# Kernel optimization log

Measured on AMD Instinct MI355X. Metric: run time of the kernel, lower is better.

Reference implementation:

```python
import jax, jax.numpy as jnp
import numpy as np
import math

A, R, E, H = 4, 2, 12, 24  # msg_angular, msg_radial, embed_dim, hidden_dim
N = A * R
B, L = 131072, 15

def _ring_adj(n):
    adj = np.zeros((n, n), np.float32)
    if n == 1:
        adj[0, 0] = 1.0
    else:
        for i in range(n):
            adj[i, (i - 1) % n] = 1.0
            adj[i, (i + 1) % n] = 1.0
    return jnp.asarray(adj)

ANG_ADJ = _ring_adj(A)
RAD_ADJ = _ring_adj(R)

def setup_inputs():
    key = jax.random.key(0)
    ks = jax.random.split(key, 16)
    p = lambda k, s: jax.random.normal(k, s, jnp.float32) * 0.1
    return {
        "x": jax.random.normal(ks[0], (B, L, 4), jnp.float32),
        "enc_w1": p(ks[1], (4, H)), "enc_b1": p(ks[2], (H,)),
        "enc_w2": p(ks[3], (H, H)), "enc_b2": p(ks[4], (H,)),
        "enc_w3": p(ks[5], (H, 3)), "enc_b3": p(ks[6], (3,)),
        "node_w1": p(ks[7], (E, H)), "node_b1": p(ks[8], (H,)),
        "node_w2": p(ks[9], (H, E)), "node_b2": p(ks[10], (E,)),
        "angular_logit": jnp.zeros((A,), jnp.float32),
        "radial_logit": jnp.zeros((R,), jnp.float32),
        "read_w1": p(ks[11], (E * N, H)), "read_b1": p(ks[12], (H,)),
        "read_w2": p(ks[13], (H, 4)), "read_b2": p(ks[14], (4,)),
    }

def _norm_adj(logit, adj):
    a = jax.nn.softmax(logit)[None, :] * adj
    return a / jnp.maximum(a.sum(1, keepdims=True), 1e-6)

def _forward(x, enc_w1, enc_b1, enc_w2, enc_b2, enc_w3, enc_b3,
             node_w1, node_b1, node_w2, node_b2,
             angular_logit, radial_logit,
             read_w1, read_b1, read_w2, read_b2):
    b = x.shape[0]
    # encoder: original loops over all timesteps but only uses the last z
    zt = jnp.tanh(x[:, -1, :] @ enc_w1 + enc_b1)
    zt = jnp.tanh(zt @ enc_w2 + enc_b2)
    z = zt @ enc_w3 + enc_b3                       # [B, 3]
    r = jax.nn.sigmoid(z[:, 0]) * (R - 1)          # R_idx in [0, R-1]
    p = (z[:, 1] + math.pi) / (2 * math.pi) * A    # phi_idx (can be <0 or >A)
    # torch code calls .item(), detaching indices/weights from autograd
    r = jax.lax.stop_gradient(r)
    p = jax.lax.stop_gradient(p)
    r0 = jnp.trunc(r)   # int() truncates toward zero
    p0 = jnp.trunc(p)
    dr = (r - r0)[:, None]
    dp = (p - p0)[:, None]
    dro = jnp.array([0.0, 0.0, 1.0, 1.0], jnp.float32)   # 4 bilinear corners
    dpo = jnp.array([0.0, 1.0, 0.0, 1.0], jnp.float32)
    wr = jnp.where(dro == 0, 1.0 - dr, dr)               # [B, 4]
    wp = jnp.where(dpo == 0, 1.0 - dp, dp)
    w = wr * wp                                          # [B, 4]
    r_i = jnp.minimum(r0.astype(jnp.int32)[:, None] + dro.astype(jnp.int32), R - 1)
    p_i = jnp.mod(p0.astype(jnp.int32)[:, None] + dpo.astype(jnp.int32), A)
    mask = (w > 0).astype(x.dtype)[:, :, None]           # 'if weight > 0' skip
    # node_embed = pad(concat([z, weight]), E); z entries are NOT weight-scaled
    vec = jnp.concatenate([
        jnp.broadcast_to(z[:, None, :], (b, 4, 3)),
        w[:, :, None],
        jnp.zeros((b, 4, E - 4), x.dtype)], axis=-1) * mask   # [B, 4, E]
    grid = jnp.zeros((b, R, A, E), x.dtype).at[
        jnp.arange(b)[:, None], r_i, p_i].add(vec)            # scatter-add
    h = grid.reshape(b, N, E)
    ang = _norm_adj(angular_logit, ANG_ADJ)  # [A, A]
    rad = _norm_adj(radial_logit, RAD_ADJ)   # [R, R]
    # faithful to the torch .view() layout mixing (r,a,e)
    h_ang = jnp.einsum('ij,bjk->bik', ang, h.reshape(b, A, R * E)).reshape(b, N, E)
    h_rad = jnp.einsum('ij,bjk->bik', rad, h.reshape(b, R, A * E)).reshape(b, N, E)
    h = h + h_ang + h_rad
    h = jnp.tanh(h @ node_w1 + node_b1) @ node_w2 + node_b2   # node_net
    out = jnp.tanh(h.reshape(b, -1) @ read_w1 + read_b1) @ read_w2 + read_b2
    return out  # [B, 4]

def reference(x, enc_w1, enc_b1, enc_w2, enc_b2, enc_w3, enc_b3,
              node_w1, node_b1, node_w2, node_b2,
              angular_logit, radial_logit,
              read_w1, read_b1, read_w2, read_b2):
    return _forward(x, enc_w1, enc_b1, enc_w2, enc_b2, enc_w3, enc_b3,
                    node_w1, node_b1, node_w2, node_b2,
                    angular_logit, radial_logit,
                    read_w1, read_b1, read_w2, read_b2)
```

## Files before the change

kernel.cpp:

```cpp
#include <hip/hip_runtime.h>
#include <math.h>


#define PI_F 3.14159265358979323846f

__device__ __forceinline__ float fast_tanh(float v) {
    float e = __expf(2.0f * v);
    return 1.0f - 2.0f * __builtin_amdgcn_rcpf(e + 1.0f);
}

__device__ __forceinline__ float quad_sum(float x) {
    x += __int_as_float(__builtin_amdgcn_update_dpp(
             0, __float_as_int(x), 0xB1, 0xF, 0xF, true));
    x += __int_as_float(__builtin_amdgcn_update_dpp(
             0, __float_as_int(x), 0x4E, 0xF, 0xF, true));
    return x;
}

#define K1_LDS 880

extern "C" __global__ void __launch_bounds__(256, 2)
topo_k1(const float* __restrict__ x,
        const float* __restrict__ ew1, const float* __restrict__ eb1,
        const float* __restrict__ ew2, const float* __restrict__ eb2,
        const float* __restrict__ ew3, const float* __restrict__ eb3,
        const float* __restrict__ alog, const float* __restrict__ rlog,
        const float* __restrict__ nw2, const float* __restrict__ nb2,
        const float* __restrict__ rw1, const float* __restrict__ rb1,
        float* __restrict__ ws, int B)
{
    const int nb1b = (B + 255) >> 8;

    if ((int)blockIdx.x >= nb1b) {
        const int gid = ((int)blockIdx.x - nb1b) * 256 + (int)threadIdx.x;
        float* M = ws + (size_t)B * 20;
        if (gid < 4608) {
            const int cell = gid / 576, rem = gid - cell * 576;
            const int j = rem / 24, j2 = rem - j * 24;
            float s = 0.0f;
            #pragma unroll
            for (int d = 0; d < 12; ++d)
                s += nw2[j * 12 + d] * rw1[(cell * 12 + d) * 24 + j2];
            M[gid] = s;
        } else if (gid < 4632) {
            const int j2 = gid - 4608;
            float s = rb1[j2];
            for (int i = 0; i < 96; ++i)
                s += nb2[i % 12] * rw1[i * 24 + j2];
            M[4608 + j2] = s;
        }
        return;
    }

    __shared__ float wf[K1_LDS];
    const float4* wq = reinterpret_cast<const float4*>(wf);
    {
        const int tt = threadIdx.x;
        for (int i = tt; i < 24; i += 256) {
            wf[i * 8 + 0] = ew1[i];
            wf[i * 8 + 1] = ew1[24 + i];
            wf[i * 8 + 2] = ew1[48 + i];
            wf[i * 8 + 3] = ew1[72 + i];
            wf[i * 8 + 4] = eb1[i];
        }
        for (int i = tt; i < 576; i += 256) wf[192 + i] = ew2[i];
        for (int i = tt; i < 24;  i += 256) wf[768 + i] = eb2[i];
        for (int i = tt; i < 72;  i += 256) wf[792 + (i % 3) * 24 + (i / 3)] = ew3[i];
        for (int i = tt; i < 3;   i += 256) wf[864 + i] = eb3[i];
    }
    __syncthreads();

    const int b = blockIdx.x * blockDim.x + threadIdx.x;
    if (b >= B) return;

    const float4 xv = *reinterpret_cast<const float4*>(x + (size_t)b * 60 + 56);

    float a2[24];
    #pragma unroll
    for (int c = 0; c < 6; ++c) {
        float4 b4 = wq[192 / 4 + c];
        a2[c*4+0] = b4.x; a2[c*4+1] = b4.y; a2[c*4+2] = b4.z; a2[c*4+3] = b4.w;
    }
    #pragma unroll 1
    for (int k = 0; k < 24; ++k) {
        float4 p  = wq[2 * k];
        float4 p2 = wq[2 * k + 1];
        const float zk = fast_tanh(p2.x + xv.x*p.x + xv.y*p.y + xv.z*p.z + xv.w*p.w);
        const int rr = 48 + k * 6;
        float4 r0 = wq[rr+0], r1 = wq[rr+1], r2 = wq[rr+2];
        float4 r3 = wq[rr+3], r4 = wq[rr+4], r5 = wq[rr+5];
        a2[0]+=zk*r0.x; a2[1]+=zk*r0.y; a2[2]+=zk*r0.z; a2[3]+=zk*r0.w;
        a2[4]+=zk*r1.x; a2[5]+=zk*r1.y; a2[6]+=zk*r1.z; a2[7]+=zk*r1.w;
        a2[8]+=zk*r2.x; a2[9]+=zk*r2.y; a2[10]+=zk*r2.z; a2[11]+=zk*r2.w;
        a2[12]+=zk*r3.x; a2[13]+=zk*r3.y; a2[14]+=zk*r3.z; a2[15]+=zk*r3.w;
        a2[16]+=zk*r4.x; a2[17]+=zk*r4.y; a2[18]+=zk*r4.z; a2[19]+=zk*r4.w;
        a2[20]+=zk*r5.x; a2[21]+=zk*r5.y; a2[22]+=zk*r5.z; a2[23]+=zk*r5.w;
    }
    float zt2[24];
    #pragma unroll
    for (int j = 0; j < 24; ++j) zt2[j] = fast_tanh(a2[j]);

    float z0 = wf[864], z1 = wf[865], z2 = wf[866];
    #pragma unroll
    for (int c = 0; c < 6; ++c) {
        float4 v0 = wq[198 + c], v1 = wq[204 + c], v2 = wq[210 + c];
        z0 += zt2[c*4+0]*v0.x + zt2[c*4+1]*v0.y + zt2[c*4+2]*v0.z + zt2[c*4+3]*v0.w;
        z1 += zt2[c*4+0]*v1.x + zt2[c*4+1]*v1.y + zt2[c*4+2]*v1.z + zt2[c*4+3]*v1.w;
        z2 += zt2[c*4+0]*v2.x + zt2[c*4+1]*v2.y + zt2[c*4+2]*v2.z + zt2[c*4+3]*v2.w;
    }

    float ang[4][4];
    {
        float m = fmaxf(fmaxf(alog[0], alog[1]), fmaxf(alog[2], alog[3]));
        float e0 = __expf(alog[0] - m), e1 = __expf(alog[1] - m);
        float e2 = __expf(alog[2] - m), e3 = __expf(alog[3] - m);
        float s = e0 + e1 + e2 + e3;
        float sm[4] = { e0 / s, e1 / s, e2 / s, e3 / s };
        #pragma unroll
        for (int i = 0; i < 4; ++i) {
            const int jn = (i + 3) & 3, jp = (i + 1) & 3;
            float inv = 1.0f / fmaxf(sm[jn] + sm[jp], 1e-6f);
            #pragma unroll
            for (int j = 0; j < 4; ++j) {
                float adj = (j == jn || j == jp) ? 1.0f : 0.0f;
                ang[i][j] = sm[j] * adj * inv;
            }
        }
    }
    float rad[2][2];
    {
        float m = fmaxf(rlog[0], rlog[1]);
        float f0 = __expf(rlog[0] - m), f1 = __expf(rlog[1] - m);
        float fs = f0 + f1;
        float sm0 = f0 / fs, sm1 = f1 / fs;
        rad[0][0] = 0.0f; rad[0][1] = sm1 / fmaxf(sm1, 1e-6f);
        rad[1][1] = 0.0f; rad[1][0] = sm0 / fmaxf(sm0, 1e-6f);
    }

    const float r = 1.0f / (1.0f + __expf(-z0));
    const float p = (z1 + PI_F) / (2.0f * PI_F) * 4.0f;
    const float r0f = truncf(r), p0f = truncf(p);
    const float dr = r - r0f, dp = p - p0f;
    const int r0i = (int)r0f, p0i = (int)p0f;

    const float w0c = (1.0f - dr) * (1.0f - dp);
    const float w1c = (1.0f - dr) * dp;
    const float w2c = dr * (1.0f - dp);
    const float w3c = dr * dp;

    const int ri0 = min(r0i, 1);
    const int ri2 = min(r0i + 1, 1);
    const int pi0 = p0i & 3;
    const int pi1 = (p0i + 1) & 3;

    const int c0 = ri0 * 4 + pi0, c1 = ri0 * 4 + pi1;
    const int c2 = ri2 * 4 + pi0, c3 = ri2 * 4 + pi1;

    float cnt[8], wsum[8];
    #pragma unroll
    for (int n = 0; n < 8; ++n) {
        float cm = 0.0f, cw = 0.0f;
        if (c0 == n && w0c > 0.0f) { cm += 1.0f; cw += w0c; }
        if (c1 == n && w1c > 0.0f) { cm += 1.0f; cw += w1c; }
        if (c2 == n && w2c > 0.0f) { cm += 1.0f; cw += w2c; }
        if (c3 == n && w3c > 0.0f) { cm += 1.0f; cw += w3c; }
        cnt[n] = cm; wsum[n] = cw;
    }
    float mc[8], mw[8];
    #pragma unroll
    for (int n = 0; n < 8; ++n) {
        float ac = cnt[n], aw = wsum[n];
        #pragma unroll
        for (int j = 0; j < 4; ++j) {
            const float g = ang[n >> 1][j];
            ac += g * cnt[2 * j + (n & 1)];
            aw += g * wsum[2 * j + (n & 1)];
        }
        #pragma unroll
        for (int j = 0; j < 2; ++j) {
            const float g = rad[n >> 2][j];
            ac += g * cnt[4 * j + (n & 3)];
            aw += g * wsum[4 * j + (n & 3)];
        }
        mc[n] = ac; mw[n] = aw;
    }

    float* wp = ws + (size_t)b * 20;
    float4 v0; v0.x = z0;    v0.y = z1;    v0.z = z2;    v0.w = 0.0f;
    float4 v1; v1.x = mc[0]; v1.y = mc[1]; v1.z = mc[2]; v1.w = mc[3];
    float4 v2; v2.x = mc[4]; v2.y = mc[5]; v2.z = mc[6]; v2.w = mc[7];
    float4 v3; v3.x = mw[0]; v3.y = mw[1]; v3.z = mw[2]; v3.w = mw[3];
    float4 v4; v4.x = mw[4]; v4.y = mw[5]; v4.z = mw[6]; v4.w = mw[7];
    reinterpret_cast<float4*>(wp)[0] = v0;
    reinterpret_cast<float4*>(wp)[1] = v1;
    reinterpret_cast<float4*>(wp)[2] = v2;
    reinterpret_cast<float4*>(wp)[3] = v3;
    reinterpret_cast<float4*>(wp)[4] = v4;
}

#define K2_LDS 4956

extern "C" __global__ void __launch_bounds__(256)
topo_k2(const float* __restrict__ ws,
        const float* __restrict__ nw1, const float* __restrict__ nb1,
        const float* __restrict__ rw2, const float* __restrict__ rb2,
        float* __restrict__ out, int B)
{
    __shared__ float wf[K2_LDS];
    const float4* wq = reinterpret_cast<const float4*>(wf);
    {
        const int tt = threadIdx.x;
        const float* Msrc = ws + (size_t)B * 20;
        for (int i = tt; i < 4608; i += 256) {
            const int cell = i / 576, rem = i - cell * 576;
            wf[192 + cell * 580 + rem] = Msrc[i];
        }
        for (int i = tt; i < 24; i += 256) wf[4832 + i] = Msrc[4608 + i];
        for (int i = tt; i < 24; i += 256) {
            wf[i * 8 + 0] = nw1[i];
            wf[i * 8 + 1] = nw1[24 + i];
            wf[i * 8 + 2] = nw1[48 + i];
            wf[i * 8 + 3] = nw1[72 + i];
            wf[i * 8 + 4] = nb1[i];
        }
        for (int i = tt; i < 96; i += 256) wf[4856 + i] = rw2[i];
        for (int i = tt; i < 4;  i += 256) wf[4952 + i] = rb2[i];
    }
    __syncthreads();

    const int tid  = blockIdx.x * blockDim.x + threadIdx.x;
    const int lane = tid & 3;
    const int b    = tid >> 2;
    if (b >= B) return;

    const float* wp = ws + (size_t)b * 20;
    const float4 zv = *reinterpret_cast<const float4*>(wp);
    const float2 mc2 = *reinterpret_cast<const float2*>(wp + 4 + 2 * lane);
    const float2 mw2 = *reinterpret_cast<const float2*>(wp + 12 + 2 * lane);
    const float z0 = zv.x, z1 = zv.y, z2 = zv.z;
    const float mcA = mc2.x, mcB = mc2.y, mwA = mw2.x, mwB = mw2.y;

    const int mAq = 48 + (2 * lane) * 145;
    const int mBq = mAq + 145;

    float t[24];
    #pragma unroll
    for (int j = 0; j < 24; ++j) t[j] = 0.0f;

    #pragma unroll 1
    for (int j = 0; j < 24; ++j) {
        float4 pk  = wq[2 * j];
        float4 pk2 = wq[2 * j + 1];
        const float q  = z0 * pk.x + z1 * pk.y + z2 * pk.z;
        const float hA = fast_tanh(pk2.x + mcA * q + mwA * pk.w);
        const float hB = fast_tanh(pk2.x + mcB * q + mwB * pk.w);
        const int ra = mAq + j * 6, rb = mBq + j * 6;
        float4 a0 = wq[ra+0], a1 = wq[ra+1], a2v = wq[ra+2];
        float4 a3 = wq[ra+3], a4 = wq[ra+4], a5  = wq[ra+5];
        float4 b0 = wq[rb+0], b1 = wq[rb+1], b2v = wq[rb+2];
        float4 b3 = wq[rb+3], b4 = wq[rb+4], b5  = wq[rb+5];
        t[0]  += hA*a0.x  + hB*b0.x;  t[1]  += hA*a0.y  + hB*b0.y;
        t[2]  += hA*a0.z  + hB*b0.z;  t[3]  += hA*a0.w  + hB*b0.w;
        t[4]  += hA*a1.x  + hB*b1.x;  t[5]  += hA*a1.y  + hB*b1.y;
        t[6]  += hA*a1.z  + hB*b1.z;  t[7]  += hA*a1.w  + hB*b1.w;
        t[8]  += hA*a2v.x + hB*b2v.x; t[9]  += hA*a2v.y + hB*b2v.y;
        t[10] += hA*a2v.z + hB*b2v.z; t[11] += hA*a2v.w + hB*b2v.w;
        t[12] += hA*a3.x  + hB*b3.x;  t[13] += hA*a3.y  + hB*b3.y;
        t[14] += hA*a3.z  + hB*b3.z;  t[15] += hA*a3.w  + hB*b3.w;
        t[16] += hA*a4.x  + hB*b4.x;  t[17] += hA*a4.y  + hB*b4.y;
        t[18] += hA*a4.z  + hB*b4.z;  t[19] += hA*a4.w  + hB*b4.w;
        t[20] += hA*a5.x  + hB*b5.x;  t[21] += hA*a5.y  + hB*b5.y;
        t[22] += hA*a5.z  + hB*b5.z;  t[23] += hA*a5.w  + hB*b5.w;
    }

    #pragma unroll
    for (int j = 0; j < 24; ++j) t[j] = quad_sum(t[j]) + wf[4832 + j];

    float4 ob = wq[1238];
    float o0 = ob.x, o1 = ob.y, o2 = ob.z, o3 = ob.w;
    #pragma unroll
    for (int j = 0; j < 24; ++j) {
        const float tv = fast_tanh(t[j]);
        float4 rv = wq[1214 + j];
        o0 += tv * rv.x; o1 += tv * rv.y; o2 += tv * rv.z; o3 += tv * rv.w;
    }
    if (lane == 0) {
        float4 ov; ov.x = o0; ov.y = o1; ov.z = o2; ov.w = o3;
        *reinterpret_cast<float4*>(out + (size_t)b * 4) = ov;
    }
}

extern "C" __global__ void __launch_bounds__(256, 2)
topo_fused(const float* __restrict__ x,
           const float* __restrict__ ew1, const float* __restrict__ eb1,
           const float* __restrict__ ew2, const float* __restrict__ eb2,
           const float* __restrict__ ew3, const float* __restrict__ eb3,
           const float* __restrict__ nw1, const float* __restrict__ nb1,
           const float* __restrict__ nw2, const float* __restrict__ nb2,
           const float* __restrict__ alog, const float* __restrict__ rlog,
           const float* __restrict__ rw1, const float* __restrict__ rb1,
           const float* __restrict__ rw2, const float* __restrict__ rb2,
           float* __restrict__ out, int B)
{
    const int b = blockIdx.x * blockDim.x + threadIdx.x;
    if (b >= B) return;

    float ang[4][4];
    {
        float m = fmaxf(fmaxf(alog[0], alog[1]), fmaxf(alog[2], alog[3]));
        float e0 = __expf(alog[0] - m), e1 = __expf(alog[1] - m);
        float e2 = __expf(alog[2] - m), e3 = __expf(alog[3] - m);
        float s = e0 + e1 + e2 + e3;
        float sm[4] = { e0 / s, e1 / s, e2 / s, e3 / s };
        #pragma unroll
        for (int i = 0; i < 4; ++i) {
            const int jn = (i + 3) & 3, jp = (i + 1) & 3;
            float inv = 1.0f / fmaxf(sm[jn] + sm[jp], 1e-6f);
            #pragma unroll
            for (int j = 0; j < 4; ++j) {
                float adj = (j == jn || j == jp) ? 1.0f : 0.0f;
                ang[i][j] = sm[j] * adj * inv;
            }
        }
    }
    float rad[2][2];
    {
        float m = fmaxf(rlog[0], rlog[1]);
        float f0 = __expf(rlog[0] - m), f1 = __expf(rlog[1] - m);
        float fs = f0 + f1;
        float sm0 = f0 / fs, sm1 = f1 / fs;
        rad[0][0] = 0.0f; rad[0][1] = sm1 / fmaxf(sm1, 1e-6f);
        rad[1][1] = 0.0f; rad[1][0] = sm0 / fmaxf(sm0, 1e-6f);
    }

    const float4 xv = *reinterpret_cast<const float4*>(x + (size_t)b * 60 + 56);
    float zt[24];
    #pragma unroll
    for (int j = 0; j < 24; ++j) {
        float a = eb1[j];
        a += xv.x * ew1[j];
        a += xv.y * ew1[24 + j];
        a += xv.z * ew1[48 + j];
        a += xv.w * ew1[72 + j];
        zt[j] = fast_tanh(a);
    }
    float z0 = eb3[0], z1 = eb3[1], z2 = eb3[2];
    #pragma unroll
    for (int j = 0; j < 24; ++j) {
        float a = eb2[j];
        #pragma unroll
        for (int k = 0; k < 24; ++k) a += zt[k] * ew2[k * 24 + j];
        const float z2t = fast_tanh(a);
        z0 += z2t * ew3[j * 3 + 0];
        z1 += z2t * ew3[j * 3 + 1];
        z2 += z2t * ew3[j * 3 + 2];
    }

    const float r = 1.0f / (1.0f + __expf(-z0));
    const float p = (z1 + PI_F) / (2.0f * PI_F) * 4.0f;
    const float r0f = truncf(r), p0f = truncf(p);
    const float dr = r - r0f, dp = p - p0f;
    const int r0i = (int)r0f, p0i = (int)p0f;
    const float w0c = (1.0f - dr) * (1.0f - dp);
    const float w1c = (1.0f - dr) * dp;
    const float w2c = dr * (1.0f - dp);
    const float w3c = dr * dp;
    const int ri0 = min(r0i, 1);
    const int ri2 = min(r0i + 1, 1);
    const int pi0 = p0i & 3;
    const int pi1 = (p0i + 1) & 3;
    const int c0 = ri0 * 4 + pi0, c1 = ri0 * 4 + pi1;
    const int c2 = ri2 * 4 + pi0, c3 = ri2 * 4 + pi1;

    float cnt[8], wsum[8];
    #pragma unroll
    for (int n = 0; n < 8; ++n) {
        float cm = 0.0f, cw = 0.0f;
        if (c0 == n && w0c > 0.0f) { cm += 1.0f; cw += w0c; }
        if (c1 == n && w1c > 0.0f) { cm += 1.0f; cw += w1c; }
        if (c2 == n && w2c > 0.0f) { cm += 1.0f; cw += w2c; }
        if (c3 == n && w3c > 0.0f) { cm += 1.0f; cw += w3c; }
        cnt[n] = cm; wsum[n] = cw;
    }
    float mc[8], mw[8];
    #pragma unroll
    for (int n = 0; n < 8; ++n) {
        float ac = cnt[n], aw = wsum[n];
        #pragma unroll
        for (int j = 0; j < 4; ++j) {
            const float g = ang[n >> 1][j];
            ac += g * cnt[2 * j + (n & 1)];
            aw += g * wsum[2 * j + (n & 1)];
        }
        #pragma unroll
        for (int j = 0; j < 2; ++j) {
            const float g = rad[n >> 2][j];
            ac += g * cnt[4 * j + (n & 3)];
            aw += g * wsum[4 * j + (n & 3)];
        }
        mc[n] = ac; mw[n] = aw;
    }

    float t[24];
    #pragma unroll
    for (int j = 0; j < 24; ++j) t[j] = rb1[j];
    #pragma unroll
    for (int n = 0; n < 8; ++n) {
        const float f0 = mc[n] * z0, f1 = mc[n] * z1, f2 = mc[n] * z2;
        float ho[12];
        #pragma unroll
        for (int d = 0; d < 12; ++d) ho[d] = nb2[d];
        #pragma unroll
        for (int j = 0; j < 24; ++j) {
            const float hj = fast_tanh(nb1[j] + f0 * nw1[j] + f1 * nw1[24 + j]
                                       + f2 * nw1[48 + j] + mw[n] * nw1[72 + j]);
            #pragma unroll
            for (int d = 0; d < 12; ++d) ho[d] += hj * nw2[j * 12 + d];
        }
        #pragma unroll
        for (int d = 0; d < 12; ++d) {
            const int rbase = (n * 12 + d) * 24;
            #pragma unroll
            for (int j2 = 0; j2 < 24; ++j2) t[j2] += ho[d] * rw1[rbase + j2];
        }
    }

    float o0 = rb2[0], o1 = rb2[1], o2 = rb2[2], o3 = rb2[3];
    #pragma unroll
    for (int j = 0; j < 24; ++j) {
        const float tt = fast_tanh(t[j]);
        o0 += tt * rw2[j * 4 + 0];
        o1 += tt * rw2[j * 4 + 1];
        o2 += tt * rw2[j * 4 + 2];
        o3 += tt * rw2[j * 4 + 3];
    }
    float4 ov; ov.x = o0; ov.y = o1; ov.z = o2; ov.w = o3;
    *reinterpret_cast<float4*>(out + (size_t)b * 4) = ov;
}

extern "C" void kernel_launch(void* const* d_in, const int* in_sizes, int n_in,
                              void* d_out, int out_size, void* d_ws, size_t ws_size,
                              hipStream_t stream) {
    const float* x    = (const float*)d_in[0];
    const float* ew1  = (const float*)d_in[1];
    const float* eb1  = (const float*)d_in[2];
    const float* ew2  = (const float*)d_in[3];
    const float* eb2  = (const float*)d_in[4];
    const float* ew3  = (const float*)d_in[5];
    const float* eb3  = (const float*)d_in[6];
    const float* nw1  = (const float*)d_in[7];
    const float* nb1  = (const float*)d_in[8];
    const float* nw2  = (const float*)d_in[9];
    const float* nb2  = (const float*)d_in[10];
    const float* alog = (const float*)d_in[11];
    const float* rlog = (const float*)d_in[12];
    const float* rw1  = (const float*)d_in[13];
    const float* rb1  = (const float*)d_in[14];
    const float* rw2  = (const float*)d_in[15];
    const float* rb2  = (const float*)d_in[16];
    float* out = (float*)d_out;

    const int B = in_sizes[0] / 60;
    const size_t ws_needed = ((size_t)B * 20 + 4632) * sizeof(float);

    if (ws_size >= ws_needed) {
        float* ws = (float*)d_ws;
        const int nb1b = (B + 255) / 256;
        const int g1 = nb1b + 19;
        topo_k1<<<g1, 256, 0, stream>>>(x, ew1, eb1, ew2, eb2, ew3, eb3,
                                        alog, rlog, nw2, nb2, rw1, rb1, ws, B);
        const long long tot2 = (long long)B * 4;
        const int g2 = (int)((tot2 + 255) / 256);
        topo_k2<<<g2, 256, 0, stream>>>(ws, nw1, nb1, rw2, rb2, out, B);
    } else {
        const int g = (B + 255) / 256;
        topo_fused<<<g, 256, 0, stream>>>(
            x, ew1, eb1, ew2, eb2, ew3, eb3, nw1, nb1, nw2, nb2,
            alog, rlog, rw1, rb1, rw2, rb2, out, B);
    }
}
```

Baseline: 54.04 us.

## Process two batch elements per 8-thread group in k2, splitting hidden outputs

Restructures the second kernel so each group of 8 threads handles two batch elements, with each thread covering half of the 24 hidden outputs. Every LDS weight float4 now feeds FMAs for two elements, which halves LDS traffic per FMA. The final readout is combined across the two halves with a ds_swizzle xor reduction. The first kernel's encoder loop is unrolled by 2, and the new layout doubles the tanh work per thread and adds an extra cross-lane reduction.

```diff
diff --git a/kernel.cpp b/kernel.cpp
--- a/kernel.cpp
+++ b/kernel.cpp
@@ -15,6 +15,11 @@
     x += __int_as_float(__builtin_amdgcn_update_dpp(
              0, __float_as_int(x), 0x4E, 0xF, 0xF, true));
     return x;
+}
+
+__device__ __forceinline__ float xor4_sum(float x) {
+    return x + __int_as_float(
+        __builtin_amdgcn_ds_swizzle(__float_as_int(x), 0x101F));
 }
 
 #define K1_LDS 880
@@ -81,7 +86,7 @@
         float4 b4 = wq[192 / 4 + c];
         a2[c*4+0] = b4.x; a2[c*4+1] = b4.y; a2[c*4+2] = b4.z; a2[c*4+3] = b4.w;
     }
-    #pragma unroll 1
+    #pragma unroll 2
     for (int k = 0; k < 24; ++k) {
         float4 p  = wq[2 * k];
         float4 p2 = wq[2 * k + 1];
@@ -229,64 +234,94 @@
     __syncthreads();
 
     const int tid  = blockIdx.x * blockDim.x + threadIdx.x;
-    const int lane = tid & 3;
-    const int b    = tid >> 2;
-    if (b >= B) return;
-
-    const float* wp = ws + (size_t)b * 20;
-    const float4 zv = *reinterpret_cast<const float4*>(wp);
-    const float2 mc2 = *reinterpret_cast<const float2*>(wp + 4 + 2 * lane);
-    const float2 mw2 = *reinterpret_cast<const float2*>(wp + 12 + 2 * lane);
-    const float z0 = zv.x, z1 = zv.y, z2 = zv.z;
-    const float mcA = mc2.x, mcB = mc2.y, mwA = mw2.x, mwB = mw2.y;
-
-    const int mAq = 48 + (2 * lane) * 145;
-    const int mBq = mAq + 145;
-
-    float t[24];
-    #pragma unroll
-    for (int j = 0; j < 24; ++j) t[j] = 0.0f;
+    const int cp   = tid & 3;
+    const int half = (tid >> 2) & 1;
+    const int slot = tid >> 3;
+    const int nP   = (B + 1) >> 1;
+    if (slot >= nP) return;
+    const int e0  = 2 * slot;
+    const int e1s = 2 * slot + 1;
+    const int e1  = (e1s < B) ? e1s : (B - 1);
+
+    const float* wp0 = ws + (size_t)e0 * 20;
+    const float* wp1 = ws + (size_t)e1 * 20;
+    const float4 zA = *reinterpret_cast<const float4*>(wp0);
+    const float4 zB = *reinterpret_cast<const float4*>(wp1);
+    const float2 mc0 = *reinterpret_cast<const float2*>(wp0 + 4 + 2 * cp);
+    const float2 mw0 = *reinterpret_cast<const float2*>(wp0 + 12 + 2 * cp);
+    const float2 mc1 = *reinterpret_cast<const float2*>(wp1 + 4 + 2 * cp);
+    const float2 mw1 = *reinterpret_cast<const float2*>(wp1 + 12 + 2 * cp);
+
+    const int mA = 48 + (2 * cp) * 145 + half * 3;
+    const int mB = mA + 145;
+
+    float t0[12], t1[12];
+    #pragma unroll
+    for (int k = 0; k < 12; ++k) { t0[k] = 0.0f; t1[k] = 0.0f; }
 
     #pragma unroll 1
     for (int j = 0; j < 24; ++j) {
         float4 pk  = wq[2 * j];
         float4 pk2 = wq[2 * j + 1];
-        const float q  = z0 * pk.x + z1 * pk.y + z2 * pk.z;
-        const float hA = fast_tanh(pk2.x + mcA * q + mwA * pk.w);
-        const float hB = fast_tanh(pk2.x + mcB * q + mwB * pk.w);
-        const int ra = mAq + j * 6, rb = mBq + j * 6;
-        float4 a0 = wq[ra+0], a1 = wq[ra+1], a2v = wq[ra+2];
-        float4 a3 = wq[ra+3], a4 = wq[ra+4], a5  = wq[ra+5];
-        float4 b0 = wq[rb+0], b1 = wq[rb+1], b2v = wq[rb+2];
-        float4 b3 = wq[rb+3], b4 = wq[rb+4], b5  = wq[rb+5];
-        t[0]  += hA*a0.x  + hB*b0.x;  t[1]  += hA*a0.y  + hB*b0.y;
-        t[2]  += hA*a0.z  + hB*b0.z;  t[3]  += hA*a0.w  + hB*b0.w;
-        t[4]  += hA*a1.x  + hB*b1.x;  t[5]  += hA*a1.y  + hB*b1.y;
-        t[6]  += hA*a1.z  + hB*b1.z;  t[7]  += hA*a1.w  + hB*b1.w;
-        t[8]  += hA*a2v.x + hB*b2v.x; t[9]  += hA*a2v.y + hB*b2v.y;
-        t[10] += hA*a2v.z + hB*b2v.z; t[11] += hA*a2v.w + hB*b2v.w;
-        t[12] += hA*a3.x  + hB*b3.x;  t[13] += hA*a3.y  + hB*b3.y;
-        t[14] += hA*a3.z  + hB*b3.z;  t[15] += hA*a3.w  + hB*b3.w;
-        t[16] += hA*a4.x  + hB*b4.x;  t[17] += hA*a4.y  + hB*b4.y;
-        t[18] += hA*a4.z  + hB*b4.z;  t[19] += hA*a4.w  + hB*b4.w;
-        t[20] += hA*a5.x  + hB*b5.x;  t[21] += hA*a5.y  + hB*b5.y;
-        t[22] += hA*a5.z  + hB*b5.z;  t[23] += hA*a5.w  + hB*b5.w;
-    }
-
-    #pragma unroll
-    for (int j = 0; j < 24; ++j) t[j] = quad_sum(t[j]) + wf[4832 + j];
-
-    float4 ob = wq[1238];
-    float o0 = ob.x, o1 = ob.y, o2 = ob.z, o3 = ob.w;
-    #pragma unroll
-    for (int j = 0; j < 24; ++j) {
-        const float tv = fast_tanh(t[j]);
-        float4 rv = wq[1214 + j];
-        o0 += tv * rv.x; o1 += tv * rv.y; o2 += tv * rv.z; o3 += tv * rv.w;
-    }
-    if (lane == 0) {
-        float4 ov; ov.x = o0; ov.y = o1; ov.z = o2; ov.w = o3;
-        *reinterpret_cast<float4*>(out + (size_t)b * 4) = ov;
+        const float nb = pk2.x, w3 = pk.w;
+        const float q0 = zA.x * pk.x + zA.y * pk.y + zA.z * pk.z;
+        const float q1 = zB.x * pk.x + zB.y * pk.y + zB.z * pk.z;
+        const float hA0 = fast_tanh(nb + mc0.x * q0 + mw0.x * w3);
+        const float hB0 = fast_tanh(nb + mc0.y * q0 + mw0.y * w3);
+        const float hA1 = fast_tanh(nb + mc1.x * q1 + mw1.x * w3);
+        const float hB1 = fast_tanh(nb + mc1.y * q1 + mw1.y * w3);
+        const int ra = mA + j * 6, rb = mB + j * 6;
+        float4 a0 = wq[ra], a1 = wq[ra + 1], a2 = wq[ra + 2];
+        t0[0] += hA0*a0.x; t0[1] += hA0*a0.y; t0[2]  += hA0*a0.z; t0[3]  += hA0*a0.w;
+        t0[4] += hA0*a1.x; t0[5] += hA0*a1.y; t0[6]  += hA0*a1.z; t0[7]  += hA0*a1.w;
+        t0[8] += hA0*a2.x; t0[9] += hA0*a2.y; t0[10] += hA0*a2.z; t0[11] += hA0*a2.w;
+        t1[0] += hA1*a0.x; t1[1] += hA1*a0.y; t1[2]  += hA1*a0.z; t1[3]  += hA1*a0.w;
+        t1[4] += hA1*a1.x; t1[5] += hA1*a1.y; t1[6]  += hA1*a1.z; t1[7]  += hA1*a1.w;
+        t1[8] += hA1*a2.x; t1[9] += hA1*a2.y; t1[10] += hA1*a2.z; t1[11] += hA1*a2.w;
+        float4 b0 = wq[rb], b1 = wq[rb + 1], b2 = wq[rb + 2];
+        t0[0] += hB0*b0.x; t0[1] += hB0*b0.y; t0[2]  += hB0*b0.z; t0[3]  += hB0*b0.w;
+        t0[4] += hB0*b1.x; t0[5] += hB0*b1.y; t0[6]  += hB0*b1.z; t0[7]  += hB0*b1.w;
+        t0[8] += hB0*b2.x; t0[9] += hB0*b2.y; t0[10] += hB0*b2.z; t0[11] += hB0*b2.w;
+        t1[0] += hB1*b0.x; t1[1] += hB1*b0.y; t1[2]  += hB1*b0.z; t1[3]  += hB1*b0.w;
+        t1[4] += hB1*b1.x; t1[5] += hB1*b1.y; t1[6]  += hB1*b1.z; t1[7]  += hB1*b1.w;
+        t1[8] += hB1*b2.x; t1[9] += hB1*b2.y; t1[10] += hB1*b2.z; t1[11] += hB1*b2.w;
+    }
+
+    #pragma unroll
+    for (int k = 0; k < 12; ++k) {
+        t0[k] = quad_sum(t0[k]);
+        t1[k] = quad_sum(t1[k]);
+    }
+    #pragma unroll
+    for (int c = 0; c < 3; ++c) {
+        float4 ti = wq[1208 + half * 3 + c];
+        t0[c*4+0] += ti.x; t0[c*4+1] += ti.y; t0[c*4+2] += ti.z; t0[c*4+3] += ti.w;
+        t1[c*4+0] += ti.x; t1[c*4+1] += ti.y; t1[c*4+2] += ti.z; t1[c*4+3] += ti.w;
+    }
+
+    float o00 = 0.0f, o01 = 0.0f, o02 = 0.0f, o03 = 0.0f;
+    float o10 = 0.0f, o11 = 0.0f, o12 = 0.0f, o13 = 0.0f;
+    #pragma unroll
+    for (int k = 0; k < 12; ++k) {
+        const float tv0 = fast_tanh(t0[k]);
+        const float tv1 = fast_tanh(t1[k]);
+        float4 rv = wq[1214 + half * 12 + k];
+        o00 += tv0 * rv.x; o01 += tv0 * rv.y; o02 += tv0 * rv.z; o03 += tv0 * rv.w;
+        o10 += tv1 * rv.x; o11 += tv1 * rv.y; o12 += tv1 * rv.z; o13 += tv1 * rv.w;
+    }
+    o00 = xor4_sum(o00); o01 = xor4_sum(o01); o02 = xor4_sum(o02); o03 = xor4_sum(o03);
+    o10 = xor4_sum(o10); o11 = xor4_sum(o11); o12 = xor4_sum(o12); o13 = xor4_sum(o13);
+
+    if ((tid & 7) == 0) {
+        float4 ob = wq[1238];
+        float4 ovA; ovA.x = o00 + ob.x; ovA.y = o01 + ob.y;
+        ovA.z = o02 + ob.z; ovA.w = o03 + ob.w;
+        *reinterpret_cast<float4*>(out + (size_t)e0 * 4) = ovA;
+        if (e1s < B) {
+            float4 ovB; ovB.x = o10 + ob.x; ovB.y = o11 + ob.y;
+            ovB.z = o12 + ob.z; ovB.w = o13 + ob.w;
+            *reinterpret_cast<float4*>(out + (size_t)e1s * 4) = ovB;
+        }
     }
 }
 
@@ -469,7 +504,8 @@
         const int g1 = nb1b + 19;
         topo_k1<<<g1, 256, 0, stream>>>(x, ew1, eb1, ew2, eb2, ew3, eb3,
                                         alog, rlog, nw2, nb2, rw1, rb1, ws, B);
-        const long long tot2 = (long long)B * 4;
+        const long long nP = ((long long)B + 1) / 2;
+        const long long tot2 = nP * 8;
         const int g2 = (int)((tot2 + 255) / 256);
         topo_k2<<<g2, 256, 0, stream>>>(ws, nw1, nb1, rw2, rb2, out, B);
     } else {
```

New measurement: 55.76 us. +3.2%, slower.

## Use one thread per sample in k2 with uniform global weight reads, pack k1 FMAs

Applied to the files above, without the earlier changes.

The second kernel drops the four-lanes-per-sample split with DPP quad reduction and LDS weight staging. Each thread now handles one sample across all 8 cells, reading a precomputed fused weight table from global memory at wave-uniform addresses. The first kernel's auxiliary blocks build that table with node_net first-layer weights interleaved into 32-wide records, and they accumulate in double precision. The encoder hidden layer uses packed two-wide FMAs with an unroll of 2. The change removes LDS staging, syncthreads and cross-lane shuffles, at the cost of four times the per-thread work and reliance on scalar or cached loads for the weights.

```diff
diff --git a/kernel.cpp b/kernel.cpp
--- a/kernel.cpp
+++ b/kernel.cpp
@@ -3,18 +3,17 @@
 
 
 #define PI_F 3.14159265358979323846f
+
+typedef float f32x2 __attribute__((ext_vector_type(2)));
+
+__device__ __forceinline__ f32x2 b2(float v) { f32x2 r; r.x = v; r.y = v; return r; }
+__device__ __forceinline__ f32x2 pkfma(f32x2 a, f32x2 b, f32x2 c) {
+    return __builtin_elementwise_fma(a, b, c);
+}
 
 __device__ __forceinline__ float fast_tanh(float v) {
     float e = __expf(2.0f * v);
     return 1.0f - 2.0f * __builtin_amdgcn_rcpf(e + 1.0f);
-}
-
-__device__ __forceinline__ float quad_sum(float x) {
-    x += __int_as_float(__builtin_amdgcn_update_dpp(
-             0, __float_as_int(x), 0xB1, 0xF, 0xF, true));
-    x += __int_as_float(__builtin_amdgcn_update_dpp(
-             0, __float_as_int(x), 0x4E, 0xF, 0xF, true));
-    return x;
 }
 
 #define K1_LDS 880
@@ -25,6 +24,7 @@
         const float* __restrict__ ew2, const float* __restrict__ eb2,
         const float* __restrict__ ew3, const float* __restrict__ eb3,
         const float* __restrict__ alog, const float* __restrict__ rlog,
+        const float* __restrict__ nw1, const float* __restrict__ nb1,
         const float* __restrict__ nw2, const float* __restrict__ nb2,
         const float* __restrict__ rw1, const float* __restrict__ rb1,
         float* __restrict__ ws, int B)
@@ -34,20 +34,28 @@
     if ((int)blockIdx.x >= nb1b) {
         const int gid = ((int)blockIdx.x - nb1b) * 256 + (int)threadIdx.x;
         float* M = ws + (size_t)B * 20;
-        if (gid < 4608) {
-            const int cell = gid / 576, rem = gid - cell * 576;
-            const int j = rem / 24, j2 = rem - j * 24;
-            float s = 0.0f;
-            #pragma unroll
-            for (int d = 0; d < 12; ++d)
-                s += nw2[j * 12 + d] * rw1[(cell * 12 + d) * 24 + j2];
-            M[gid] = s;
-        } else if (gid < 4632) {
-            const int j2 = gid - 4608;
-            float s = rb1[j2];
+        if (gid < 6144) {
+            const int r = gid >> 5, c = gid & 31;
+            const int cell = r / 24, j = r - cell * 24;
+            float v = 0.0f;
+            if (c < 24) {
+                double s = 0.0;
+                #pragma unroll
+                for (int d = 0; d < 12; ++d)
+                    s += (double)nw2[j * 12 + d] * (double)rw1[(cell * 12 + d) * 24 + c];
+                v = (float)s;
+            } else if (c == 24) v = nb1[j];
+            else if (c == 25) v = nw1[72 + j];
+            else if (c == 26) v = nw1[j];
+            else if (c == 27) v = nw1[24 + j];
+            else if (c == 28) v = nw1[48 + j];
+            M[gid] = v;
+        } else if (gid < 6168) {
+            const int j2 = gid - 6144;
+            double s = (double)rb1[j2];
             for (int i = 0; i < 96; ++i)
-                s += nb2[i % 12] * rw1[i * 24 + j2];
-            M[4608 + j2] = s;
+                s += (double)nb2[i % 12] * (double)rw1[i * 24 + j2];
+            M[6144 + j2] = (float)s;
         }
         return;
     }
@@ -75,30 +83,33 @@
 
     const float4 xv = *reinterpret_cast<const float4*>(x + (size_t)b * 60 + 56);
 
-    float a2[24];
+    f32x2 A2[12];
     #pragma unroll
     for (int c = 0; c < 6; ++c) {
         float4 b4 = wq[192 / 4 + c];
-        a2[c*4+0] = b4.x; a2[c*4+1] = b4.y; a2[c*4+2] = b4.z; a2[c*4+3] = b4.w;
-    }
-    #pragma unroll 1
+        A2[c*2+0].x = b4.x; A2[c*2+0].y = b4.y;
+        A2[c*2+1].x = b4.z; A2[c*2+1].y = b4.w;
+    }
+    #pragma unroll 2
     for (int k = 0; k < 24; ++k) {
         float4 p  = wq[2 * k];
         float4 p2 = wq[2 * k + 1];
         const float zk = fast_tanh(p2.x + xv.x*p.x + xv.y*p.y + xv.z*p.z + xv.w*p.w);
+        const f32x2 zk2 = b2(zk);
         const int rr = 48 + k * 6;
-        float4 r0 = wq[rr+0], r1 = wq[rr+1], r2 = wq[rr+2];
-        float4 r3 = wq[rr+3], r4 = wq[rr+4], r5 = wq[rr+5];
-        a2[0]+=zk*r0.x; a2[1]+=zk*r0.y; a2[2]+=zk*r0.z; a2[3]+=zk*r0.w;
-        a2[4]+=zk*r1.x; a2[5]+=zk*r1.y; a2[6]+=zk*r1.z; a2[7]+=zk*r1.w;
-        a2[8]+=zk*r2.x; a2[9]+=zk*r2.y; a2[10]+=zk*r2.z; a2[11]+=zk*r2.w;
-        a2[12]+=zk*r3.x; a2[13]+=zk*r3.y; a2[14]+=zk*r3.z; a2[15]+=zk*r3.w;
-        a2[16]+=zk*r4.x; a2[17]+=zk*r4.y; a2[18]+=zk*r4.z; a2[19]+=zk*r4.w;
-        a2[20]+=zk*r5.x; a2[21]+=zk*r5.y; a2[22]+=zk*r5.z; a2[23]+=zk*r5.w;
+        #pragma unroll
+        for (int c = 0; c < 6; ++c) {
+            float4 rv = wq[rr + c];
+            f32x2 r01; r01.x = rv.x; r01.y = rv.y;
+            f32x2 r23; r23.x = rv.z; r23.y = rv.w;
+            A2[c*2+0] = pkfma(zk2, r01, A2[c*2+0]);
+            A2[c*2+1] = pkfma(zk2, r23, A2[c*2+1]);
+        }
     }
     float zt2[24];
     #pragma unroll
-    for (int j = 0; j < 24; ++j) zt2[j] = fast_tanh(a2[j]);
+    for (int j = 0; j < 24; ++j)
+        zt2[j] = fast_tanh((j & 1) ? A2[j >> 1].y : A2[j >> 1].x);
 
     float z0 = wf[864], z1 = wf[865], z2 = wf[866];
     #pragma unroll
@@ -198,96 +209,58 @@
     reinterpret_cast<float4*>(wp)[4] = v4;
 }
 
-#define K2_LDS 4956
-
 extern "C" __global__ void __launch_bounds__(256)
 topo_k2(const float* __restrict__ ws,
-        const float* __restrict__ nw1, const float* __restrict__ nb1,
         const float* __restrict__ rw2, const float* __restrict__ rb2,
         float* __restrict__ out, int B)
 {
-    __shared__ float wf[K2_LDS];
-    const float4* wq = reinterpret_cast<const float4*>(wf);
-    {
-        const int tt = threadIdx.x;
-        const float* Msrc = ws + (size_t)B * 20;
-        for (int i = tt; i < 4608; i += 256) {
-            const int cell = i / 576, rem = i - cell * 576;
-            wf[192 + cell * 580 + rem] = Msrc[i];
-        }
-        for (int i = tt; i < 24; i += 256) wf[4832 + i] = Msrc[4608 + i];
-        for (int i = tt; i < 24; i += 256) {
-            wf[i * 8 + 0] = nw1[i];
-            wf[i * 8 + 1] = nw1[24 + i];
-            wf[i * 8 + 2] = nw1[48 + i];
-            wf[i * 8 + 3] = nw1[72 + i];
-            wf[i * 8 + 4] = nb1[i];
-        }
-        for (int i = tt; i < 96; i += 256) wf[4856 + i] = rw2[i];
-        for (int i = tt; i < 4;  i += 256) wf[4952 + i] = rb2[i];
-    }
-    __syncthreads();
-
-    const int tid  = blockIdx.x * blockDim.x + threadIdx.x;
-    const int lane = tid & 3;
-    const int b    = tid >> 2;
+    const int b = blockIdx.x * blockDim.x + threadIdx.x;
     if (b >= B) return;
 
+    const float* __restrict__ Ms = ws + (size_t)B * 20;
+    const float* __restrict__ ti = Ms + 6144;
+
     const float* wp = ws + (size_t)b * 20;
-    const float4 zv = *reinterpret_cast<const float4*>(wp);
-    const float2 mc2 = *reinterpret_cast<const float2*>(wp + 4 + 2 * lane);
-    const float2 mw2 = *reinterpret_cast<const float2*>(wp + 12 + 2 * lane);
+    const float4 zv  = reinterpret_cast<const float4*>(wp)[0];
+    const float4 mcv0 = reinterpret_cast<const float4*>(wp)[1];
+    const float4 mcv1 = reinterpret_cast<const float4*>(wp)[2];
+    const float4 mwv0 = reinterpret_cast<const float4*>(wp)[3];
+    const float4 mwv1 = reinterpret_cast<const float4*>(wp)[4];
+    const float mc[8] = { mcv0.x, mcv0.y, mcv0.z, mcv0.w,
+                          mcv1.x, mcv1.y, mcv1.z, mcv1.w };
+    const float mw[8] = { mwv0.x, mwv0.y, mwv0.z, mwv0.w,
+                          mwv1.x, mwv1.y, mwv1.z, mwv1.w };
     const float z0 = zv.x, z1 = zv.y, z2 = zv.z;
-    const float mcA = mc2.x, mcB = mc2.y, mwA = mw2.x, mwB = mw2.y;
-
-    const int mAq = 48 + (2 * lane) * 145;
-    const int mBq = mAq + 145;
 
     float t[24];
     #pragma unroll
-    for (int j = 0; j < 24; ++j) t[j] = 0.0f;
-
-    #pragma unroll 1
+    for (int k = 0; k < 24; ++k) t[k] = ti[k];
+
+    #pragma unroll
+    for (int cell = 0; cell < 8; ++cell) {
+        const float mcc = mc[cell], mwc = mw[cell];
+        const float* __restrict__ rc = Ms + cell * 768;
+        #pragma unroll 1
+        for (int j = 0; j < 24; ++j) {
+            const float* __restrict__ rec = rc + (j << 5);
+            const float q = z0 * rec[26] + z1 * rec[27] + z2 * rec[28];
+            const float h = fast_tanh(rec[24] + mcc * q + mwc * rec[25]);
+            #pragma unroll
+            for (int k = 0; k < 24; ++k) t[k] = fmaf(h, rec[k], t[k]);
+        }
+    }
+
+    float o0 = rb2[0], o1 = rb2[1], o2 = rb2[2], o3 = rb2[3];
+    #pragma unroll
     for (int j = 0; j < 24; ++j) {
-        float4 pk  = wq[2 * j];
-        float4 pk2 = wq[2 * j + 1];
-        const float q  = z0 * pk.x + z1 * pk.y + z2 * pk.z;
-        const float hA = fast_tanh(pk2.x + mcA * q + mwA * pk.w);
-        const float hB = fast_tanh(pk2.x + mcB * q + mwB * pk.w);
-        const int ra = mAq + j * 6, rb = mBq + j * 6;
-        float4 a0 = wq[ra+0], a1 = wq[ra+1], a2v = wq[ra+2];
-        float4 a3 = wq[ra+3], a4 = wq[ra+4], a5  = wq[ra+5];
-        float4 b0 = wq[rb+0], b1 = wq[rb+1], b2v = wq[rb+2];
-        float4 b3 = wq[rb+3], b4 = wq[rb+4], b5  = wq[rb+5];
-        t[0]  += hA*a0.x  + hB*b0.x;  t[1]  += hA*a0.y  + hB*b0.y;
-        t[2]  += hA*a0.z  + hB*b0.z;  t[3]  += hA*a0.w  + hB*b0.w;
-        t[4]  += hA*a1.x  + hB*b1.x;  t[5]  += hA*a1.y  + hB*b1.y;
-        t[6]  += hA*a1.z  + hB*b1.z;  t[7]  += hA*a1.w  + hB*b1.w;
-        t[8]  += hA*a2v.x + hB*b2v.x; t[9]  += hA*a2v.y + hB*b2v.y;
-        t[10] += hA*a2v.z + hB*b2v.z; t[11] += hA*a2v.w + hB*b2v.w;
-        t[12] += hA*a3.x  + hB*b3.x;  t[13] += hA*a3.y  + hB*b3.y;
-        t[14] += hA*a3.z  + hB*b3.z;  t[15] += hA*a3.w  + hB*b3.w;
-        t[16] += hA*a4.x  + hB*b4.x;  t[17] += hA*a4.y  + hB*b4.y;
-        t[18] += hA*a4.z  + hB*b4.z;  t[19] += hA*a4.w  + hB*b4.w;
-        t[20] += hA*a5.x  + hB*b5.x;  t[21] += hA*a5.y  + hB*b5.y;
-        t[22] += hA*a5.z  + hB*b5.z;  t[23] += hA*a5.w  + hB*b5.w;
-    }
-
-    #pragma unroll
-    for (int j = 0; j < 24; ++j) t[j] = quad_sum(t[j]) + wf[4832 + j];
-
-    float4 ob = wq[1238];
-    float o0 = ob.x, o1 = ob.y, o2 = ob.z, o3 = ob.w;
-    #pragma unroll
-    for (int j = 0; j < 24; ++j) {
-        const float tv = fast_tanh(t[j]);
-        float4 rv = wq[1214 + j];
-        o0 += tv * rv.x; o1 += tv * rv.y; o2 += tv * rv.z; o3 += tv * rv.w;
-    }
-    if (lane == 0) {
-        float4 ov; ov.x = o0; ov.y = o1; ov.z = o2; ov.w = o3;
-        *reinterpret_cast<float4*>(out + (size_t)b * 4) = ov;
-    }
+        const float tt = fast_tanh(t[j]);
+        o0 = fmaf(tt, rw2[j * 4 + 0], o0);
+        o1 = fmaf(tt, rw2[j * 4 + 1], o1);
+        o2 = fmaf(tt, rw2[j * 4 + 2], o2);
+        o3 = fmaf(tt, rw2[j * 4 + 3], o3);
+    }
+    float4 ov; ov.x = o0; ov.y = o1; ov.z = o2; ov.w = o3;
+    *reinterpret_cast<float4*>(out + (size_t)b * 4) = ov;
 }
 
 extern "C" __global__ void __launch_bounds__(256, 2)
@@ -461,17 +434,17 @@
     float* out = (float*)d_out;
 
     const int B = in_sizes[0] / 60;
-    const size_t ws_needed = ((size_t)B * 20 + 4632) * sizeof(float);
+    const size_t ws_needed = ((size_t)B * 20 + 6168) * sizeof(float);
 
     if (ws_size >= ws_needed) {
         float* ws = (float*)d_ws;
         const int nb1b = (B + 255) / 256;
-        const int g1 = nb1b + 19;
+        const int g1 = nb1b + 25;
         topo_k1<<<g1, 256, 0, stream>>>(x, ew1, eb1, ew2, eb2, ew3, eb3,
-                                        alog, rlog, nw2, nb2, rw1, rb1, ws, B);
-        const long long tot2 = (long long)B * 4;
-        const int g2 = (int)((tot2 + 255) / 256);
-        topo_k2<<<g2, 256, 0, stream>>>(ws, nw1, nb1, rw2, rb2, out, B);
+                                        alog, rlog, nw1, nb1, nw2, nb2,
+                                        rw1, rb1, ws, B);
+        const int g2 = (B + 255) / 256;
+        topo_k2<<<g2, 256, 0, stream>>>(ws, rw2, rb2, out, B);
     } else {
         const int g = (B + 255) / 256;
         topo_fused<<<g, 256, 0, stream>>>(
```

New measurement: 78.02 us. 44.4% more time.
